# Performance work log

Measured on AMD Instinct MI355X. Metric: run time of the kernel, lower is better.

Reference implementation:

```python
import jax, jax.numpy as jnp
import numpy as np

M, K, N = 8192, 4096, 11008  # tokens, in_features, out_features


def setup_inputs() -> dict:
    key = jax.random.key(0)
    k1, k2, k3 = jax.random.split(key, 3)
    x = jax.random.normal(k1, (M, K), dtype=jnp.float16)
    # Build realistic int8 weights + per-output-channel scales by quantizing
    # a kaiming-like fp32 weight (mirrors quantize_weight_per_channel).
    w_fp32 = jax.random.normal(k2, (N, K), dtype=jnp.float32) * 0.02
    weight_scale = jnp.max(jnp.abs(w_fp32), axis=1) / 127.0  # [N] float32
    weight_int8 = jnp.clip(jnp.round(w_fp32 / weight_scale[:, None]), -127, 127).astype(jnp.int8)
    bias = jax.random.normal(k3, (N,), dtype=jnp.float32) * 0.01
    return {"x": x, "weight_int8": weight_int8, "weight_scale": weight_scale, "bias": bias}


def reference(x, weight_int8, weight_scale, bias):
    # W8A16 GEMM with fused per-output-channel dequant + bias.
    # Per-row scale commutes with the K-contraction, so apply it post-accumulation
    # (exactly what the fused Triton kernel does). Accumulate in fp32.
    w = weight_int8.astype(jnp.float16)  # [N, K]
    acc = jnp.einsum('mk,nk->mn', x, w, preferred_element_type=jnp.float32)  # [M, N] fp32
    out = acc * weight_scale[None, :] + bias[None, :]
    return out.astype(x.dtype)
```

## Files before the change

### kernel.cpp

```cpp
#include <hip/hip_runtime.h>
#include <hip/hip_fp16.h>


#define M_DIM 8192
#define K_DIM 4096
#define N_DIM 11008

#define TM 128
#define TN 128
#define BK 64
#define BKP 72

#define MT_TILES 32
#define NT_TILES 43
#define NWG (MT_TILES * NT_TILES)
#define CPX (NWG / 8)

typedef __attribute__((ext_vector_type(8))) _Float16 half8;
typedef __attribute__((ext_vector_type(4))) float floatx4;

union Pack16 { int4 i4; unsigned short u[8]; _Float16 h[8]; };

__global__ __launch_bounds__(256) void probe_w(const int* __restrict__ W,
                                               unsigned int* __restrict__ f) {
    const size_t i0 = (size_t)blockIdx.x * 256 + threadIdx.x;
    const size_t stride = (size_t)gridDim.x * 256;
    int bad = 0;
    for (size_t i = i0; i < (size_t)(1u << 20); i += stride) {
        int w = W[i];
        if (w > 127 || w < -127) bad = 1;
    }
    if (bad) atomicOr(f, 1u);
}

__global__ __launch_bounds__(256) void convert_x(const float* __restrict__ Xf,
                                                 unsigned short* __restrict__ Xh) {
    const size_t i = ((size_t)blockIdx.x * 256 + threadIdx.x) * 8;
    float4 a = *(const float4*)(Xf + i);
    float4 b = *(const float4*)(Xf + i + 4);
    Pack16 p;
    p.h[0] = (_Float16)a.x; p.h[1] = (_Float16)a.y;
    p.h[2] = (_Float16)a.z; p.h[3] = (_Float16)a.w;
    p.h[4] = (_Float16)b.x; p.h[5] = (_Float16)b.y;
    p.h[6] = (_Float16)b.z; p.h[7] = (_Float16)b.w;
    *(int4*)(Xh + i) = p.i4;
}

__global__ __launch_bounds__(256) void convert_w(const void* __restrict__ Wraw,
                                                 unsigned short* __restrict__ Wh,
                                                 const unsigned int* __restrict__ f) {
    const bool w8 = f[0] != 0u;
    const size_t i = ((size_t)blockIdx.x * 256 + threadIdx.x) * 8;
    int v[8];
    if (w8) {
        int2 b = *(const int2*)((const char*)Wraw + i);
#pragma unroll
        for (int j = 0; j < 4; ++j)
            v[j] = (int)(signed char)(unsigned char)((((unsigned)b.x) >> (8 * j)) & 0xFFu);
#pragma unroll
        for (int j = 0; j < 4; ++j)
            v[4 + j] = (int)(signed char)(unsigned char)((((unsigned)b.y) >> (8 * j)) & 0xFFu);
    } else {
        const int4* src = (const int4*)((const int*)Wraw + i);
        int4 w0 = src[0], w1 = src[1];
        v[0] = w0.x; v[1] = w0.y; v[2] = w0.z; v[3] = w0.w;
        v[4] = w1.x; v[5] = w1.y; v[6] = w1.z; v[7] = w1.w;
    }
    Pack16 p;
#pragma unroll
    for (int j = 0; j < 8; ++j) p.h[j] = (_Float16)v[j];
    *(int4*)(Wh + i) = p.i4;
}


__device__ __forceinline__ void gl16(const void* g, void* l) {
    __builtin_amdgcn_global_load_lds(
        (const __attribute__((address_space(1))) unsigned int*)g,
        (__attribute__((address_space(3))) unsigned int*)l, 16, 0, 0);
}

__global__ __launch_bounds__(512, 2) void w8a16_gemm_8ph(
    const unsigned short* __restrict__ Xh, const unsigned short* __restrict__ Wh,
    const float* __restrict__ scale, const float* __restrict__ bias,
    float* __restrict__ Out)
{
    __shared__ unsigned char lds[2][2][2][16384];

    const int t = threadIdx.x;
    const int lane = t & 63;
    const int wv = t >> 6;
    const int wr = wv >> 2;
    const int wc = wv & 3;
    const int fr = lane & 15;
    const int q  = lane >> 4;

    const int bid = blockIdx.x;
    const int swz = (bid & 7) * CPX + (bid >> 3);
    const int mt = swz / NT_TILES;
    const int nt = swz - mt * NT_TILES;
    const size_t tileM = (size_t)mt << 8;
    const size_t tileN = (size_t)nt << 8;

    const int rr = t >> 2;
    const int cA = ((((t & 3) << 4) ^ (((t >> 2) & 6) << 3)) >> 1);
    const unsigned short* srcA0 = Xh + (tileM + rr) * K_DIM + cA;
    const unsigned short* srcA1 = srcA0 + (size_t)128 * K_DIM;
    const unsigned short* srcB0 = Wh + (tileN + rr) * K_DIM + cA;
    const unsigned short* srcB1 = srcB0 + (size_t)128 * K_DIM;
    const int wvofs = wv << 10;

    const int gsw = (fr & 6) << 3;
    const int rdA = ((((wr << 7) + fr) << 6) + (q << 4)) ^ gsw;
    const int rdB = ((((wc << 6) + fr) << 6) + (q << 4)) ^ gsw;

    floatx4 acc[8][4];
#pragma unroll
    for (int m = 0; m < 8; ++m)
#pragma unroll
        for (int n = 0; n < 4; ++n) acc[m][n] = (floatx4){0.f, 0.f, 0.f, 0.f};

    half8 afrag[4], bfrag[4];

#define STAGE_A(d_, kh_, tau_) do { \
    const unsigned short* _g0 = srcA0 + ((tau_) * 64 + (kh_) * 32); \
    const unsigned short* _g1 = srcA1 + ((tau_) * 64 + (kh_) * 32); \
    unsigned char* _l = &lds[d_][0][kh_][0] + wvofs; \
    gl16(_g0, _l); gl16(_g1, _l + 8192); \
} while (0)

#define STAGE_B(d_, kh_, tau_) do { \
    const unsigned short* _g0 = srcB0 + ((tau_) * 64 + (kh_) * 32); \
    const unsigned short* _g1 = srcB1 + ((tau_) * 64 + (kh_) * 32); \
    unsigned char* _l = &lds[d_][1][kh_][0] + wvofs; \
    gl16(_g0, _l); gl16(_g1, _l + 8192); \
} while (0)

#define VM4 asm volatile("s_waitcnt vmcnt(4)" ::: "memory")
#define VM0 asm volatile("s_waitcnt vmcnt(0)" ::: "memory")
#define NOSTG ((void)0)

#define PHASE(d_, kh_, mg_, RB_, STG_, VM_) do { \
    const unsigned char* _Ab = &lds[d_][0][kh_][0]; \
    const unsigned char* _Bb = &lds[d_][1][kh_][0]; \
    if (RB_) { \
        _Pragma("unroll") \
        for (int _n = 0; _n < 4; ++_n) \
            bfrag[_n] = *(const half8*)(const void*)(_Bb + rdB + _n * 1024); \
    } \
    _Pragma("unroll") \
    for (int _m = 0; _m < 4; ++_m) \
        afrag[_m] = *(const half8*)(const void*)(_Ab + rdA + (mg_) * 4096 + _m * 1024); \
    STG_; \
    VM_; \
    asm volatile("s_barrier" ::: "memory"); \
    asm volatile("s_waitcnt lgkmcnt(0)" ::: "memory"); \
    __builtin_amdgcn_sched_barrier(0); \
    __builtin_amdgcn_s_setprio(1); \
    _Pragma("unroll") \
    for (int _m = 0; _m < 4; ++_m) \
        _Pragma("unroll") \
        for (int _n = 0; _n < 4; ++_n) \
            acc[(mg_) * 4 + _m][_n] = __builtin_amdgcn_mfma_f32_16x16x32_f16( \
                afrag[_m], bfrag[_n], acc[(mg_) * 4 + _m][_n], 0, 0, 0); \
    __builtin_amdgcn_s_setprio(0); \
    asm volatile("s_barrier" ::: "memory"); \
} while (0)

    STAGE_A(0, 0, 0); STAGE_B(0, 0, 0); STAGE_A(0, 1, 0); STAGE_B(0, 1, 0);
    STAGE_A(1, 0, 1); STAGE_B(1, 0, 1);
    asm volatile("s_waitcnt vmcnt(4)" ::: "memory");
    asm volatile("s_barrier" ::: "memory");

#pragma unroll 1
    for (int i = 0; i < 31; ++i) {
        const int t1 = 2 * i + 1, u0 = 2 * i + 2, u1 = 2 * i + 3;
        PHASE(0, 0, 0, 1, STAGE_A(1, 1, t1), NOSTG);
        PHASE(0, 0, 1, 0, STAGE_B(1, 1, t1), NOSTG);
        PHASE(0, 1, 0, 1, STAGE_A(0, 0, u0), NOSTG);
        PHASE(0, 1, 1, 0, STAGE_B(0, 0, u0), VM4);
        PHASE(1, 0, 0, 1, STAGE_A(0, 1, u0), NOSTG);
        PHASE(1, 0, 1, 0, STAGE_B(0, 1, u0), NOSTG);
        PHASE(1, 1, 0, 1, STAGE_A(1, 0, u1), NOSTG);
        PHASE(1, 1, 1, 0, STAGE_B(1, 0, u1), VM4);
    }
    PHASE(0, 0, 0, 1, STAGE_A(1, 1, 63), NOSTG);
    PHASE(0, 0, 1, 0, STAGE_B(1, 1, 63), NOSTG);
    PHASE(0, 1, 0, 1, NOSTG, NOSTG);
    PHASE(0, 1, 1, 0, NOSTG, VM0);
    PHASE(1, 0, 0, 1, NOSTG, NOSTG);
    PHASE(1, 0, 1, 0, NOSTG, NOSTG);
    PHASE(1, 1, 0, 1, NOSTG, NOSTG);
    PHASE(1, 1, 1, 0, NOSTG, NOSTG);

#undef PHASE
#undef STAGE_A
#undef STAGE_B
#undef VM4
#undef VM0
#undef NOSTG

    const int rbase = q << 2;
#pragma unroll
    for (int ni = 0; ni < 4; ++ni) {
        const int n = (int)tileN + (wc << 6) + (ni << 4) + fr;
        const float s = scale[n];
        const float bz = bias[n];
#pragma unroll
        for (int mi = 0; mi < 8; ++mi) {
            const size_t m = tileM + (size_t)((wr << 7) + (mi << 4) + rbase);
#pragma unroll
            for (int r = 0; r < 4; ++r)
                Out[(m + r) * N_DIM + n] = acc[mi][ni][r] * s + bz;
        }
    }
}

template <bool XPRE, bool WPRE>
__global__ __launch_bounds__(256) void w8a16_gemm(
    const float* __restrict__ Xf, const unsigned short* __restrict__ Xh,
    const int* __restrict__ Wi, const unsigned short* __restrict__ Wh,
    const float* __restrict__ scale, const float* __restrict__ bias,
    float* __restrict__ Out)
{
    __shared__ unsigned short As[TM * BKP];
    __shared__ unsigned short Bs[TN * BKP];

    const int t = threadIdx.x;
    const int lane = t & 63;
    const int wave = t >> 6;
    const int tileM = blockIdx.y * TM;
    const int tileN = blockIdx.x * TN;
    const int wm = (wave & 1) * 64;
    const int wn = (wave >> 1) * 64;
    const int fr = lane & 15;
    const int fk = (lane >> 4) * 8;

    floatx4 acc[4][4];
#pragma unroll
    for (int mi = 0; mi < 4; ++mi)
#pragma unroll
        for (int ni = 0; ni < 4; ++ni) acc[mi][ni] = (floatx4){0.f, 0.f, 0.f, 0.f};

    for (int k0 = 0; k0 < K_DIM; k0 += BK) {
#pragma unroll
        for (int it = 0; it < 4; ++it) {
            const int c = it * 256 + t;
            const int r = c >> 3;
            const int qq = c & 7;
            if (XPRE) {
                *(int4*)(As + r * BKP + qq * 8) =
                    *(const int4*)(Xh + (size_t)(tileM + r) * K_DIM + k0 + qq * 8);
            } else {
                const float* s = Xf + (size_t)(tileM + r) * K_DIM + k0 + qq * 8;
                float4 x0 = ((const float4*)s)[0];
                float4 x1 = ((const float4*)s)[1];
                Pack16 p;
                p.h[0] = (_Float16)x0.x; p.h[1] = (_Float16)x0.y;
                p.h[2] = (_Float16)x0.z; p.h[3] = (_Float16)x0.w;
                p.h[4] = (_Float16)x1.x; p.h[5] = (_Float16)x1.y;
                p.h[6] = (_Float16)x1.z; p.h[7] = (_Float16)x1.w;
                *(int4*)(As + r * BKP + qq * 8) = p.i4;
            }
            if (WPRE) {
                *(int4*)(Bs + r * BKP + qq * 8) =
                    *(const int4*)(Wh + (size_t)(tileN + r) * K_DIM + k0 + qq * 8);
            } else {
                const int* s = Wi + (size_t)(tileN + r) * K_DIM + k0 + qq * 8;
                int4 w0 = ((const int4*)s)[0];
                int4 w1 = ((const int4*)s)[1];
                Pack16 p;
                p.h[0] = (_Float16)w0.x; p.h[1] = (_Float16)w0.y;
                p.h[2] = (_Float16)w0.z; p.h[3] = (_Float16)w0.w;
                p.h[4] = (_Float16)w1.x; p.h[5] = (_Float16)w1.y;
                p.h[6] = (_Float16)w1.z; p.h[7] = (_Float16)w1.w;
                *(int4*)(Bs + r * BKP + qq * 8) = p.i4;
            }
        }
        __syncthreads();
#pragma unroll
        for (int kh = 0; kh < 2; ++kh) {
            half8 a[4], b[4];
#pragma unroll
            for (int i = 0; i < 4; ++i)
                a[i] = *(const half8*)(const void*)(As + (wm + i * 16 + fr) * BKP + kh * 32 + fk);
#pragma unroll
            for (int i = 0; i < 4; ++i)
                b[i] = *(const half8*)(const void*)(Bs + (wn + i * 16 + fr) * BKP + kh * 32 + fk);
#pragma unroll
            for (int mi = 0; mi < 4; ++mi)
#pragma unroll
                for (int ni = 0; ni < 4; ++ni)
                    acc[mi][ni] = __builtin_amdgcn_mfma_f32_16x16x32_f16(
                        a[mi], b[ni], acc[mi][ni], 0, 0, 0);
        }
        __syncthreads();
    }

    const int rbase = (lane >> 4) * 4;
#pragma unroll
    for (int ni = 0; ni < 4; ++ni) {
        const int n = tileN + wn + ni * 16 + fr;
        const float s = scale[n];
        const float bz = bias[n];
#pragma unroll
        for (int mi = 0; mi < 4; ++mi) {
            const int m = tileM + wm + mi * 16 + rbase;
#pragma unroll
            for (int r = 0; r < 4; ++r)
                Out[(size_t)(m + r) * N_DIM + n] = acc[mi][ni][r] * s + bz;
        }
    }
}

extern "C" void kernel_launch(void* const* d_in, const int* in_sizes, int n_in,
                              void* d_out, int out_size, void* d_ws, size_t ws_size,
                              hipStream_t stream) {
    const long long SZ_X = (long long)M_DIM * K_DIM;
    const long long SZ_W = (long long)N_DIM * K_DIM;
    const void *pX = nullptr, *pW = nullptr, *pS = nullptr, *pB = nullptr;
    int smallIdx[8];
    int nSmall = 0;
    for (int i = 0; i < n_in; ++i) {
        long long s = in_sizes[i];
        if (s == SZ_X && !pX) pX = d_in[i];
        else if (s == SZ_W && !pW) pW = d_in[i];
        else if (s == (long long)N_DIM && nSmall < 8) smallIdx[nSmall++] = i;
    }
    if (nSmall == 2) {
        if (smallIdx[0] == 2)      { pS = d_in[2]; pB = d_in[smallIdx[1]]; }
        else if (smallIdx[1] == 2) { pS = d_in[2]; pB = d_in[smallIdx[0]]; }
        else                       { pS = d_in[smallIdx[0]]; pB = d_in[smallIdx[1]]; }
    }
    if (!pX || !pW || !pS || !pB) { pX = d_in[0]; pW = d_in[1]; pS = d_in[2]; pB = d_in[3]; }

    const float* Xf = (const float*)pX;
    const int* Wi = (const int*)pW;
    const float* scale = (const float*)pS;
    const float* bias = (const float*)pB;
    float* Out = (float*)d_out;

    dim3 gridOld(N_DIM / TN, M_DIM / TM);
    const size_t OFF = 256;
    const size_t XH_BYTES = (size_t)SZ_X * 2;
    const size_t WH_BYTES = (size_t)SZ_W * 2;

    if (ws_size >= OFF + XH_BYTES + WH_BYTES + 64) {
        unsigned int* flags = (unsigned int*)d_ws;
        unsigned short* Xh = (unsigned short*)((char*)d_ws + OFF);
        unsigned short* Wh = (unsigned short*)((char*)d_ws + OFF + XH_BYTES);
        hipMemsetAsync(flags, 0, 4, stream);
        probe_w<<<256, 256, 0, stream>>>(Wi, flags);
        convert_x<<<(int)(SZ_X / 8 / 256), 256, 0, stream>>>(Xf, Xh);
        convert_w<<<(int)(SZ_W / 8 / 256), 256, 0, stream>>>(pW, Wh, flags);
        w8a16_gemm_8ph<<<dim3(NWG), dim3(512), 0, stream>>>(Xh, Wh, scale, bias, Out);
    } else if (ws_size >= OFF + WH_BYTES + 64) {
        unsigned int* flags = (unsigned int*)d_ws;
        unsigned short* Wh = (unsigned short*)((char*)d_ws + OFF);
        hipMemsetAsync(flags, 0, 4, stream);
        probe_w<<<256, 256, 0, stream>>>(Wi, flags);
        convert_w<<<(int)(SZ_W / 8 / 256), 256, 0, stream>>>(pW, Wh, flags);
        w8a16_gemm<false, true><<<gridOld, 256, 0, stream>>>(Xf, nullptr, Wi, Wh, scale, bias, Out);
    } else {
        w8a16_gemm<false, false><<<gridOld, 256, 0, stream>>>(Xf, nullptr, Wi, nullptr, scale, bias, Out);
    }
}
```

Before: 1.213 ms.

## Prefetch B tiles one phase earlier, swap MFMA operands for vectorized stores

Reorders the global-to-LDS staging so the B half-tiles are issued a phase earlier, with one extra B load in the prologue, and relaxes the vmcnt waits from 4 to 6 to keep more loads in flight. It drops the explicit lgkmcnt(0) wait before the MFMAs and lets the compiler place LDS waits instead. It swaps the A/B operands of the MFMA so each lane holds four consecutive output columns, which allows float4 scale/bias loads and 16-byte output stores in the epilogue. The deeper prefetch relies on the LDS buffer slots being free at the new issue points, which is a race risk if the ordering is wrong.

Result: slower. 1.238 ms (+2.1%).

```diff
diff --git a/kernel.cpp b/kernel.cpp
--- a/kernel.cpp
+++ b/kernel.cpp
@@ -135,7 +135,7 @@
     gl16(_g0, _l); gl16(_g1, _l + 8192); \
 } while (0)
 
-#define VM4 asm volatile("s_waitcnt vmcnt(4)" ::: "memory")
+#define VM6 asm volatile("s_waitcnt vmcnt(6)" ::: "memory")
 #define VM0 asm volatile("s_waitcnt vmcnt(0)" ::: "memory")
 #define NOSTG ((void)0)
 
@@ -153,38 +153,37 @@
     STG_; \
     VM_; \
     asm volatile("s_barrier" ::: "memory"); \
-    asm volatile("s_waitcnt lgkmcnt(0)" ::: "memory"); \
-    __builtin_amdgcn_sched_barrier(0); \
     __builtin_amdgcn_s_setprio(1); \
     _Pragma("unroll") \
     for (int _m = 0; _m < 4; ++_m) \
         _Pragma("unroll") \
         for (int _n = 0; _n < 4; ++_n) \
             acc[(mg_) * 4 + _m][_n] = __builtin_amdgcn_mfma_f32_16x16x32_f16( \
-                afrag[_m], bfrag[_n], acc[(mg_) * 4 + _m][_n], 0, 0, 0); \
+                bfrag[_n], afrag[_m], acc[(mg_) * 4 + _m][_n], 0, 0, 0); \
     __builtin_amdgcn_s_setprio(0); \
+    __builtin_amdgcn_sched_barrier(0); \
     asm volatile("s_barrier" ::: "memory"); \
 } while (0)
 
     STAGE_A(0, 0, 0); STAGE_B(0, 0, 0); STAGE_A(0, 1, 0); STAGE_B(0, 1, 0);
-    STAGE_A(1, 0, 1); STAGE_B(1, 0, 1);
-    asm volatile("s_waitcnt vmcnt(4)" ::: "memory");
+    STAGE_A(1, 0, 1); STAGE_B(1, 0, 1); STAGE_B(1, 1, 1);
+    asm volatile("s_waitcnt vmcnt(6)" ::: "memory");
     asm volatile("s_barrier" ::: "memory");
 
 #pragma unroll 1
     for (int i = 0; i < 31; ++i) {
         const int t1 = 2 * i + 1, u0 = 2 * i + 2, u1 = 2 * i + 3;
         PHASE(0, 0, 0, 1, STAGE_A(1, 1, t1), NOSTG);
-        PHASE(0, 0, 1, 0, STAGE_B(1, 1, t1), NOSTG);
+        PHASE(0, 0, 1, 0, STAGE_B(0, 0, u0), NOSTG);
         PHASE(0, 1, 0, 1, STAGE_A(0, 0, u0), NOSTG);
-        PHASE(0, 1, 1, 0, STAGE_B(0, 0, u0), VM4);
+        PHASE(0, 1, 1, 0, STAGE_B(0, 1, u0), VM6);
         PHASE(1, 0, 0, 1, STAGE_A(0, 1, u0), NOSTG);
-        PHASE(1, 0, 1, 0, STAGE_B(0, 1, u0), NOSTG);
+        PHASE(1, 0, 1, 0, STAGE_B(1, 0, u1), NOSTG);
         PHASE(1, 1, 0, 1, STAGE_A(1, 0, u1), NOSTG);
-        PHASE(1, 1, 1, 0, STAGE_B(1, 0, u1), VM4);
+        PHASE(1, 1, 1, 0, STAGE_B(1, 1, u1), VM6);
     }
     PHASE(0, 0, 0, 1, STAGE_A(1, 1, 63), NOSTG);
-    PHASE(0, 0, 1, 0, STAGE_B(1, 1, 63), NOSTG);
+    PHASE(0, 0, 1, 0, NOSTG, NOSTG);
     PHASE(0, 1, 0, 1, NOSTG, NOSTG);
     PHASE(0, 1, 1, 0, NOSTG, VM0);
     PHASE(1, 0, 0, 1, NOSTG, NOSTG);
@@ -195,22 +194,25 @@
 #undef PHASE
 #undef STAGE_A
 #undef STAGE_B
-#undef VM4
+#undef VM6
 #undef VM0
 #undef NOSTG
 
-    const int rbase = q << 2;
+    const int q4 = q << 2;
 #pragma unroll
     for (int ni = 0; ni < 4; ++ni) {
-        const int n = (int)tileN + (wc << 6) + (ni << 4) + fr;
-        const float s = scale[n];
-        const float bz = bias[n];
+        const int nb = (int)tileN + (wc << 6) + (ni << 4) + q4;
+        const float4 s4 = *(const float4*)(scale + nb);
+        const float4 b4 = *(const float4*)(bias + nb);
 #pragma unroll
         for (int mi = 0; mi < 8; ++mi) {
-            const size_t m = tileM + (size_t)((wr << 7) + (mi << 4) + rbase);
-#pragma unroll
-            for (int r = 0; r < 4; ++r)
-                Out[(m + r) * N_DIM + n] = acc[mi][ni][r] * s + bz;
+            const size_t m = tileM + (size_t)((wr << 7) + (mi << 4) + fr);
+            float4 o;
+            o.x = acc[mi][ni][0] * s4.x + b4.x;
+            o.y = acc[mi][ni][1] * s4.y + b4.y;
+            o.z = acc[mi][ni][2] * s4.z + b4.z;
+            o.w = acc[mi][ni][3] * s4.w + b4.w;
+            *(float4*)(Out + m * N_DIM + nb) = o;
         }
     }
 }
```

## Switch GEMM inner loop to 32x32x16 MFMA with swapped operands and vectorized epilogue

Applied to the files above, without the earlier changes.

Replaces the 16x16x32 f16 MFMA tiling with 32x32x16 MFMA instructions, reorganizing LDS fragment reads into two K-halves per 32-row fragment. The B and A operands are swapped so each lane's accumulator holds consecutive output columns, which lets the epilogue write float4 stores and read scale and bias as float4. The larger MFMA is meant to cut instruction count and LDS reads per FLOP. The risk is different LDS bank-conflict behaviour from the new read addressing, plus the changed accumulator layout.

After: 1.321 ms. 8.9% more time.

```diff
diff --git a/kernel.cpp b/kernel.cpp
--- a/kernel.cpp
+++ b/kernel.cpp
@@ -18,6 +18,7 @@
 
 typedef __attribute__((ext_vector_type(8))) _Float16 half8;
 typedef __attribute__((ext_vector_type(4))) float floatx4;
+typedef __attribute__((ext_vector_type(16))) float floatx16;
 
 union Pack16 { int4 i4; unsigned short u[8]; _Float16 h[8]; };
 
@@ -91,8 +92,8 @@
     const int wv = t >> 6;
     const int wr = wv >> 2;
     const int wc = wv & 3;
-    const int fr = lane & 15;
-    const int q  = lane >> 4;
+    const int fr32 = lane & 31;
+    const int h = lane >> 5;
 
     const int bid = blockIdx.x;
     const int swz = (bid & 7) * CPX + (bid >> 3);
@@ -109,17 +110,21 @@
     const unsigned short* srcB1 = srcB0 + (size_t)128 * K_DIM;
     const int wvofs = wv << 10;
 
-    const int gsw = (fr & 6) << 3;
-    const int rdA = ((((wr << 7) + fr) << 6) + (q << 4)) ^ gsw;
-    const int rdB = ((((wc << 6) + fr) << 6) + (q << 4)) ^ gsw;
-
-    floatx4 acc[8][4];
-#pragma unroll
-    for (int m = 0; m < 8; ++m)
-#pragma unroll
-        for (int n = 0; n < 4; ++n) acc[m][n] = (floatx4){0.f, 0.f, 0.f, 0.f};
-
-    half8 afrag[4], bfrag[4];
+    const int gswz = (fr32 & 6) << 3;
+    const int rdA  = (((wr << 7) + fr32) << 6) + ((h << 4) ^ gswz);
+    const int rdA2 = rdA ^ 32;
+    const int rdB  = (((wc << 6) + fr32) << 6) + ((h << 4) ^ gswz);
+    const int rdB2 = rdB ^ 32;
+
+    floatx16 acc[4][2];
+#pragma unroll
+    for (int m = 0; m < 4; ++m)
+#pragma unroll
+        for (int n = 0; n < 2; ++n)
+            acc[m][n] = (floatx16){0.f,0.f,0.f,0.f,0.f,0.f,0.f,0.f,
+                                   0.f,0.f,0.f,0.f,0.f,0.f,0.f,0.f};
+
+    half8 afr[2][2], bfr[2][2];
 
 #define STAGE_A(d_, kh_, tau_) do { \
     const unsigned short* _g0 = srcA0 + ((tau_) * 64 + (kh_) * 32); \
@@ -144,12 +149,16 @@
     const unsigned char* _Bb = &lds[d_][1][kh_][0]; \
     if (RB_) { \
         _Pragma("unroll") \
-        for (int _n = 0; _n < 4; ++_n) \
-            bfrag[_n] = *(const half8*)(const void*)(_Bb + rdB + _n * 1024); \
+        for (int _n = 0; _n < 2; ++_n) { \
+            bfr[_n][0] = *(const half8*)(const void*)(_Bb + rdB  + _n * 2048); \
+            bfr[_n][1] = *(const half8*)(const void*)(_Bb + rdB2 + _n * 2048); \
+        } \
     } \
     _Pragma("unroll") \
-    for (int _m = 0; _m < 4; ++_m) \
-        afrag[_m] = *(const half8*)(const void*)(_Ab + rdA + (mg_) * 4096 + _m * 1024); \
+    for (int _m = 0; _m < 2; ++_m) { \
+        afr[_m][0] = *(const half8*)(const void*)(_Ab + rdA  + (mg_) * 4096 + _m * 2048); \
+        afr[_m][1] = *(const half8*)(const void*)(_Ab + rdA2 + (mg_) * 4096 + _m * 2048); \
+    } \
     STG_; \
     VM_; \
     asm volatile("s_barrier" ::: "memory"); \
@@ -157,11 +166,13 @@
     __builtin_amdgcn_sched_barrier(0); \
     __builtin_amdgcn_s_setprio(1); \
     _Pragma("unroll") \
-    for (int _m = 0; _m < 4; ++_m) \
+    for (int _m = 0; _m < 2; ++_m) \
         _Pragma("unroll") \
-        for (int _n = 0; _n < 4; ++_n) \
-            acc[(mg_) * 4 + _m][_n] = __builtin_amdgcn_mfma_f32_16x16x32_f16( \
-                afrag[_m], bfrag[_n], acc[(mg_) * 4 + _m][_n], 0, 0, 0); \
+        for (int _n = 0; _n < 2; ++_n) \
+            _Pragma("unroll") \
+            for (int _k = 0; _k < 2; ++_k) \
+                acc[(mg_) * 2 + _m][_n] = __builtin_amdgcn_mfma_f32_32x32x16_f16( \
+                    bfr[_n][_k], afr[_m][_k], acc[(mg_) * 2 + _m][_n], 0, 0, 0); \
     __builtin_amdgcn_s_setprio(0); \
     asm volatile("s_barrier" ::: "memory"); \
 } while (0)
@@ -199,18 +210,25 @@
 #undef VM0
 #undef NOSTG
 
-    const int rbase = q << 2;
-#pragma unroll
-    for (int ni = 0; ni < 4; ++ni) {
-        const int n = (int)tileN + (wc << 6) + (ni << 4) + fr;
-        const float s = scale[n];
-        const float bz = bias[n];
-#pragma unroll
-        for (int mi = 0; mi < 8; ++mi) {
-            const size_t m = tileM + (size_t)((wr << 7) + (mi << 4) + rbase);
-#pragma unroll
-            for (int r = 0; r < 4; ++r)
-                Out[(m + r) * N_DIM + n] = acc[mi][ni][r] * s + bz;
+    const int h4 = h << 2;
+#pragma unroll
+    for (int mt2 = 0; mt2 < 4; ++mt2) {
+        const size_t m = tileM + (size_t)((wr << 7) + (mt2 << 5) + fr32);
+        float* orow = Out + m * N_DIM;
+#pragma unroll
+        for (int ntt = 0; ntt < 2; ++ntt) {
+#pragma unroll
+            for (int g = 0; g < 4; ++g) {
+                const int nb = (int)tileN + (wc << 6) + (ntt << 5) + (g << 3) + h4;
+                const float4 s4 = *(const float4*)(scale + nb);
+                const float4 b4 = *(const float4*)(bias + nb);
+                float4 o;
+                o.x = acc[mt2][ntt][g * 4 + 0] * s4.x + b4.x;
+                o.y = acc[mt2][ntt][g * 4 + 1] * s4.y + b4.y;
+                o.z = acc[mt2][ntt][g * 4 + 2] * s4.z + b4.z;
+                o.w = acc[mt2][ntt][g * 4 + 3] * s4.w + b4.w;
+                *(float4*)(orow + nb) = o;
+            }
         }
     }
 }
```

## Software-pipeline LDS fragment reads one phase ahead of MFMA compute

Applied to the files above, without the earlier changes.

Splits each phase into separate LDS-read, wait and MFMA steps, and double-buffers the A/B register fragments. The next phase's fragments are read while the current phase's MFMAs run, with partial lgkmcnt waits instead of a full drain. This targets the LDS read latency that used to sit exposed before each MFMA block. In exchange it uses more VGPRs for the extra fragment buffers and depends on careful barrier and waitcnt ordering. It also adds a stray unused label.

Measured after the change: 1.234 ms. No clear change (+1.7%).

```diff
diff --git a/kernel.cpp b/kernel.cpp
--- a/kernel.cpp
+++ b/kernel.cpp
@@ -119,7 +119,7 @@
 #pragma unroll
         for (int n = 0; n < 4; ++n) acc[m][n] = (floatx4){0.f, 0.f, 0.f, 0.f};
 
-    half8 afrag[4], bfrag[4];
+    half8 a0[4], a1[4], b0f[4], b1f[4];
 
 #define STAGE_A(d_, kh_, tau_) do { \
     const unsigned short* _g0 = srcA0 + ((tau_) * 64 + (kh_) * 32); \
@@ -137,67 +137,75 @@
 
 #define VM4 asm volatile("s_waitcnt vmcnt(4)" ::: "memory")
 #define VM0 asm volatile("s_waitcnt vmcnt(0)" ::: "memory")
+#define BAR asm volatile("s_barrier" ::: "memory")
 #define NOSTG ((void)0)
 
-#define PHASE(d_, kh_, mg_, RB_, STG_, VM_) do { \
+#define RD(d_, kh_, mg_, RB_, A_, B_) do { \
     const unsigned char* _Ab = &lds[d_][0][kh_][0]; \
-    const unsigned char* _Bb = &lds[d_][1][kh_][0]; \
     if (RB_) { \
+        const unsigned char* _Bb = &lds[d_][1][kh_][0]; \
         _Pragma("unroll") \
         for (int _n = 0; _n < 4; ++_n) \
-            bfrag[_n] = *(const half8*)(const void*)(_Bb + rdB + _n * 1024); \
+            B_[_n] = *(const half8*)(const void*)(_Bb + rdB + _n * 1024); \
     } \
     _Pragma("unroll") \
     for (int _m = 0; _m < 4; ++_m) \
-        afrag[_m] = *(const half8*)(const void*)(_Ab + rdA + (mg_) * 4096 + _m * 1024); \
-    STG_; \
-    VM_; \
-    asm volatile("s_barrier" ::: "memory"); \
-    asm volatile("s_waitcnt lgkmcnt(0)" ::: "memory"); \
+        A_[_m] = *(const half8*)(const void*)(_Ab + rdA + (mg_) * 4096 + _m * 1024); \
+} while (0)
+
+#define LG(n_) do { \
+    asm volatile("s_waitcnt lgkmcnt(" #n_ ")" ::: "memory"); \
     __builtin_amdgcn_sched_barrier(0); \
+} while (0)
+
+#define MM(mg_, A_, B_) do { \
     __builtin_amdgcn_s_setprio(1); \
     _Pragma("unroll") \
     for (int _m = 0; _m < 4; ++_m) \
         _Pragma("unroll") \
         for (int _n = 0; _n < 4; ++_n) \
             acc[(mg_) * 4 + _m][_n] = __builtin_amdgcn_mfma_f32_16x16x32_f16( \
-                afrag[_m], bfrag[_n], acc[(mg_) * 4 + _m][_n], 0, 0, 0); \
+                A_[_m], B_[_n], acc[(mg_) * 4 + _m][_n], 0, 0, 0); \
     __builtin_amdgcn_s_setprio(0); \
-    asm volatile("s_barrier" ::: "memory"); \
 } while (0)
 
     STAGE_A(0, 0, 0); STAGE_B(0, 0, 0); STAGE_A(0, 1, 0); STAGE_B(0, 1, 0);
     STAGE_A(1, 0, 1); STAGE_B(1, 0, 1);
     asm volatile("s_waitcnt vmcnt(4)" ::: "memory");
-    asm volatile("s_barrier" ::: "memory");
+    BAR;
+    RD(0, 0, 0, 1, a1, b0f);
 
 #pragma unroll 1
     for (int i = 0; i < 31; ++i) {
         const int t1 = 2 * i + 1, u0 = 2 * i + 2, u1 = 2 * i + 3;
-        PHASE(0, 0, 0, 1, STAGE_A(1, 1, t1), NOSTG);
-        PHASE(0, 0, 1, 0, STAGE_B(1, 1, t1), NOSTG);
-        PHASE(0, 1, 0, 1, STAGE_A(0, 0, u0), NOSTG);
-        PHASE(0, 1, 1, 0, STAGE_B(0, 0, u0), VM4);
-        PHASE(1, 0, 0, 1, STAGE_A(0, 1, u0), NOSTG);
-        PHASE(1, 0, 1, 0, STAGE_B(0, 1, u0), NOSTG);
-        PHASE(1, 1, 0, 1, STAGE_A(1, 0, u1), NOSTG);
-        PHASE(1, 1, 1, 0, STAGE_B(1, 0, u1), VM4);
-    }
-    PHASE(0, 0, 0, 1, STAGE_A(1, 1, 63), NOSTG);
-    PHASE(0, 0, 1, 0, STAGE_B(1, 1, 63), NOSTG);
-    PHASE(0, 1, 0, 1, NOSTG, NOSTG);
-    PHASE(0, 1, 1, 0, NOSTG, VM0);
-    PHASE(1, 0, 0, 1, NOSTG, NOSTG);
-    PHASE(1, 0, 1, 0, NOSTG, NOSTG);
-    PHASE(1, 1, 0, 1, NOSTG, NOSTG);
-    PHASE(1, 1, 1, 0, NOSTG, NOSTG);
-
-#undef PHASE
+        STAGE_A(1, 1, t1); BAR; RD(0, 0, 1, 0, a0, b0f); LG(4); MM(0, a1, b0f); BAR;
+        STAGE_B(1, 1, t1); BAR; RD(0, 1, 0, 1, a1, b1f); LG(8); MM(1, a0, b0f); BAR;
+        STAGE_A(0, 0, u0); BAR; RD(0, 1, 1, 0, a0, b1f); LG(4); MM(0, a1, b1f); BAR;
+        STAGE_B(0, 0, u0); VM4; BAR; RD(1, 0, 0, 1, a1, b0f); LG(8); MM(1, a0, b1f); BAR;
+        STAGE_A(0, 1, u0); BAR; RD(1, 0, 1, 0, a0, b0f); LG(4); MM(0, a1, b0f); BAR;
+        STAGE_B(0, 1, u0); BAR; RD(1, 1, 0, 1, a1, b1f); LG(8); MM(1, a0, b0f); BAR;
+        STAGE_A(1, 0, u1); BAR; RD(1, 1, 1, 0, a0, b1f); LG(4); MM(0, a1, b1f); BAR;
+        STAGE_B(1, 0, u1); VM4; BAR; RD(0, 0, 0, 1, a1, b0f); LG(8); MM(1, a0, b1f); BAR;
+    }
+    STAGE_A(1, 1, 63); BAR; RD(0, 0, 1, 0, a0, b0f); LG(4); MM(0, a1, b0f); BAR;
+    STAGE_B(1, 1, 63); BAR; RD(0, 1, 0, 1, a1, b1f); LG(8); MM(1, a0, b0f); BAR;
+    BAR_SPLIT_P3: ;
+    BAR; RD(0, 1, 1, 0, a0, b1f); LG(4); MM(0, a1, b1f); BAR;
+    VM0; BAR; RD(1, 0, 0, 1, a1, b0f); LG(8); MM(1, a0, b1f); BAR;
+    BAR; RD(1, 0, 1, 0, a0, b0f); LG(4); MM(0, a1, b0f); BAR;
+    BAR; RD(1, 1, 0, 1, a1, b1f); LG(8); MM(1, a0, b0f); BAR;
+    BAR; RD(1, 1, 1, 0, a0, b1f); LG(4); MM(0, a1, b1f); BAR;
+    BAR; LG(0); MM(1, a0, b1f); BAR;
+
 #undef STAGE_A
 #undef STAGE_B
 #undef VM4
 #undef VM0
+#undef BAR
 #undef NOSTG
+#undef RD
+#undef LG
+#undef MM
 
     const int rbase = q << 2;
 #pragma unroll
```
